# Performance work log

Hardware: AMD Instinct MI355X
Metric: run time of the kernel (lower is better)

## Reference

```python
import jax, jax.numpy as jnp
import numpy as np

N = 50000        # nodes
E = 1_600_000    # edges
IN = 64          # in_feats
H = 128          # h_feats
L = 5            # num_layers
G = 512          # graphs in batch
C = 10           # num_classes


def setup_inputs() -> dict:
    key = jax.random.key(0)
    ks = jax.random.split(key, 12)
    s = 0.05
    x = jax.random.normal(ks[0], (N, IN), jnp.float32)
    edge_index = jax.random.randint(ks[1], (2, E), 0, N, dtype=jnp.int32)
    batch = jnp.sort(jax.random.randint(ks[2], (N,), 0, G, dtype=jnp.int32))
    edge_weight = jax.random.uniform(ks[3], (E,), jnp.float32)
    # GatedGraphConv params: per-layer mixing weight + shared GRUCell
    weight = jax.random.normal(ks[4], (L, H, H), jnp.float32) * s
    w_ih = jax.random.normal(ks[5], (3 * H, H), jnp.float32) * s
    w_hh = jax.random.normal(ks[6], (3 * H, H), jnp.float32) * s
    b_ih = jax.random.normal(ks[7], (3 * H,), jnp.float32) * s
    b_hh = jax.random.normal(ks[8], (3 * H,), jnp.float32) * s
    # MLP head
    dense1_w = jax.random.normal(ks[9], (4 * H, H), jnp.float32) * s
    dense1_b = jnp.zeros((4 * H,), jnp.float32)
    dense2_w = jax.random.normal(ks[10], (C, 4 * H), jnp.float32) * s
    dense2_b = jnp.zeros((C,), jnp.float32)
    return dict(x=x, edge_index=edge_index, batch=batch, edge_weight=edge_weight,
                weight=weight, w_ih=w_ih, w_hh=w_hh, b_ih=b_ih, b_hh=b_hh,
                dense1_w=dense1_w, dense1_b=dense1_b,
                dense2_w=dense2_w, dense2_b=dense2_b)


def _gru_cell(m, h, w_ih, w_hh, b_ih, b_hh):
    # torch.nn.GRUCell(input=m, hidden=h)
    gi = m @ w_ih.T + b_ih
    gh = h @ w_hh.T + b_hh
    i_r, i_z, i_n = jnp.split(gi, 3, axis=-1)
    h_r, h_z, h_n = jnp.split(gh, 3, axis=-1)
    r = jax.nn.sigmoid(i_r + h_r)
    z = jax.nn.sigmoid(i_z + h_z)
    n = jnp.tanh(i_n + r * h_n)
    return (1.0 - z) * n + z * h


def reference(x, edge_index, batch, edge_weight, weight, w_ih, w_hh, b_ih, b_hh,
              dense1_w, dense1_b, dense2_w, dense2_b):
    src, dst = edge_index[0], edge_index[1]
    # pad in_feats -> h_feats (PyG GatedGraphConv)
    h = jnp.pad(x, ((0, 0), (0, H - IN)))
    for l in range(L):
        m = h @ weight[l]                          # [N, H]
        msg = m[src] * edge_weight[:, None]        # gather + edge gating [E, H]
        agg = jax.ops.segment_sum(msg, dst, num_segments=N)  # scatter-add
        h = _gru_cell(agg, h, w_ih, w_hh, b_ih, b_hh)
    pooled = jax.ops.segment_max(h, batch, num_segments=G)   # global max pool [G, H]
    # dropout is identity in eval mode
    hid = jax.nn.relu(pooled @ dense1_w.T + dense1_b)
    out = hid @ dense2_w.T + dense2_b
    return out
```

## Files before the change

### kernel.cpp

```cpp
#include <hip/hip_runtime.h>
#include <hip/hip_bf16.h>

#define NN 50000
#define NE 1600000
#define FIN 64
#define H 128
#define NL 5
#define NG 512
#define NC 10

typedef __attribute__((ext_vector_type(8))) short short8;
typedef __attribute__((ext_vector_type(4))) float f32x4;

#define OFF_H2A   0
#define OFF_H2B   3200000
#define OFF_CUR   6400000
#define OFF_OFF   6450176
#define OFF_CSR   6500352
#define OFF_POOL  8900352
#define OFF_FWF   8965888
#define OFF_FWHH  9088768

__device__ __forceinline__ short rne_bf16(float f){
    unsigned u = __float_as_uint(f);
    unsigned r = (u + 0x7FFFu + ((u >> 16) & 1u)) >> 16;
    return (short)r;
}
__device__ __forceinline__ float bf_lo(unsigned v){ return __uint_as_float(v << 16); }
__device__ __forceinline__ float bf_hi(unsigned v){ return __uint_as_float(v & 0xFFFF0000u); }


__global__ void k_hist(const int* __restrict__ ei, int* __restrict__ cnt){
    int e0 = (blockIdx.x*256 + threadIdx.x)*4;
    if (e0 + 3 < NE){
        int4 d = *(const int4*)(ei + NE + e0);
        atomicAdd(&cnt[d.x], 1); atomicAdd(&cnt[d.y], 1);
        atomicAdd(&cnt[d.z], 1); atomicAdd(&cnt[d.w], 1);
    } else {
        for (int e = e0; e < NE; ++e) atomicAdd(&cnt[ei[NE + e]], 1);
    }
}

__global__ void k_scan(int* __restrict__ cur, int* __restrict__ off){
    __shared__ int s[1024];
    int t = threadIdx.x;
    const int CH = 49;
    int base = t*CH;
    int m = (NN + 1) - base; if (m > CH) m = CH; if (m < 0) m = 0;
    int sum = 0;
    for (int i = 0; i < m; ++i) sum += (cur[base + i] + 15) & ~15;
    s[t] = sum; __syncthreads();
    for (int o = 1; o < 1024; o <<= 1){
        int v = (t >= o) ? s[t - o] : 0; __syncthreads();
        s[t] += v; __syncthreads();
    }
    int run = s[t] - sum;
    for (int i = 0; i < m; ++i){
        int c = (cur[base + i] + 15) & ~15;
        off[base + i] = run;
        cur[base + i] = run;
        run += c;
    }
}

__global__ void k_fill(const int* __restrict__ ei, const float* __restrict__ ew,
                       int* __restrict__ cur, unsigned* __restrict__ csr){
    int e0 = (blockIdx.x*256 + threadIdx.x)*4;
    if (e0 + 3 < NE){
        int4   s = *(const int4*)(ei + e0);
        int4   d = *(const int4*)(ei + NE + e0);
        float4 w = *(const float4*)(ew + e0);
        int p0 = atomicAdd(&cur[d.x], 1);
        int p1 = atomicAdd(&cur[d.y], 1);
        int p2 = atomicAdd(&cur[d.z], 1);
        int p3 = atomicAdd(&cur[d.w], 1);
        csr[p0] = (unsigned)s.x | (((unsigned)(ushort)rne_bf16(w.x)) << 16);
        csr[p1] = (unsigned)s.y | (((unsigned)(ushort)rne_bf16(w.y)) << 16);
        csr[p2] = (unsigned)s.z | (((unsigned)(ushort)rne_bf16(w.z)) << 16);
        csr[p3] = (unsigned)s.w | (((unsigned)(ushort)rne_bf16(w.w)) << 16);
    } else {
        for (int e = e0; e < NE; ++e){
            int src = ei[e], dst = ei[NE + e];
            int pos = atomicAdd(&cur[dst], 1);
            csr[pos] = (unsigned)src | (((unsigned)(ushort)rne_bf16(ew[e])) << 16);
        }
    }
}


__global__ void k_pad(const float* __restrict__ x, ushort* __restrict__ h2a){
    int idx = blockIdx.x*256 + threadIdx.x;
    int n = idx >> 4, f8 = idx & 15;
    short8 v;
    if (f8 < 8){
        float4 a = *(const float4*)(x + n*FIN + f8*8);
        float4 b = *(const float4*)(x + n*FIN + f8*8 + 4);
        v[0]=rne_bf16(a.x); v[1]=rne_bf16(a.y); v[2]=rne_bf16(a.z); v[3]=rne_bf16(a.w);
        v[4]=rne_bf16(b.x); v[5]=rne_bf16(b.y); v[6]=rne_bf16(b.z); v[7]=rne_bf16(b.w);
    } else {
        v[0]=0; v[1]=0; v[2]=0; v[3]=0; v[4]=0; v[5]=0; v[6]=0; v[7]=0;
    }
    *(short8*)(h2a + idx*8) = v;
}

__global__ void k_fuse(const float* __restrict__ W, const float* __restrict__ wih,
                       short* __restrict__ fwf){
    int idx = blockIdx.x*256 + threadIdx.x;
    int l = idx / 49152;
    int r = idx % 49152;
    int k = r / 384, n = r % 384;
    const float4* wl = (const float4*)(W + l*16384 + k*128);
    const float4* wi = (const float4*)(wih + n*128);
    float acc = 0.f;
    #pragma unroll 8
    for (int c = 0; c < 32; ++c){
        float4 a = wl[c], b = wi[c];
        acc += a.x*b.x + a.y*b.y + a.z*b.z + a.w*b.w;
    }
    int lane = ((k>>3)&3)*16 + (n&15);
    fwf[l*49152 + (((n>>4)*4 + (k>>5))*64 + lane)*8 + (k&7)] = rne_bf16(acc);
}

__global__ void k_cvt_whh(const float* __restrict__ whh, short* __restrict__ fwhh){
    int idx = blockIdx.x*256 + threadIdx.x;
    int k = idx / 384, n = idx % 384;
    float v = whh[n*128 + k];
    int lane = ((k>>3)&3)*16 + (n&15);
    fwhh[(((n>>4)*4 + (k>>5))*64 + lane)*8 + (k&7)] = rne_bf16(v);
}

__global__ void k_init_pool(unsigned* __restrict__ p){
    p[blockIdx.x*256 + threadIdx.x] = 0x007FFFFFu;
}

__global__ __launch_bounds__(512)
void k_layer(const ushort* __restrict__ h2r, ushort* __restrict__ h2w,
             const int* __restrict__ off, const unsigned* __restrict__ csr,
             const short* __restrict__ fwf, const short* __restrict__ fwhh,
             const float* __restrict__ b_ih, const float* __restrict__ b_hh,
             const int* __restrict__ batch, unsigned* __restrict__ pooled,
             int last){
    __shared__ ushort tl[16*136];
    int tid = threadIdx.x;
    int n0 = blockIdx.x * 16;
    int wave = tid >> 6, lane = tid & 63;
    int lane_lo = lane & 15, quad = lane >> 4;
    int grp = lane >> 4, fl = lane & 15;

    for (int sub = 0; sub < 2; ++sub){
        int node = n0 + wave*2 + sub;
        int start = __builtin_amdgcn_readfirstlane(off[node]);
        int end   = __builtin_amdgcn_readfirstlane(off[node + 1]);
        float a0=0.f,a1=0.f,a2=0.f,a3=0.f,a4=0.f,a5=0.f,a6=0.f,a7=0.f;
        const ushort* hb = h2r + fl*8;
        for (int i = start; i < end; i += 16){
            uint4 c = *(const uint4*)(csr + i + grp*4);
            uint4 v0 = *(const uint4*)(hb + (c.x & 0xFFFFu)*H);
            uint4 v1 = *(const uint4*)(hb + (c.y & 0xFFFFu)*H);
            uint4 v2 = *(const uint4*)(hb + (c.z & 0xFFFFu)*H);
            uint4 v3 = *(const uint4*)(hb + (c.w & 0xFFFFu)*H);
            float w0 = bf_hi(c.x), w1 = bf_hi(c.y), w2 = bf_hi(c.z), w3 = bf_hi(c.w);
            a0 += w0*bf_lo(v0.x); a1 += w0*bf_hi(v0.x); a2 += w0*bf_lo(v0.y); a3 += w0*bf_hi(v0.y);
            a4 += w0*bf_lo(v0.z); a5 += w0*bf_hi(v0.z); a6 += w0*bf_lo(v0.w); a7 += w0*bf_hi(v0.w);
            a0 += w1*bf_lo(v1.x); a1 += w1*bf_hi(v1.x); a2 += w1*bf_lo(v1.y); a3 += w1*bf_hi(v1.y);
            a4 += w1*bf_lo(v1.z); a5 += w1*bf_hi(v1.z); a6 += w1*bf_lo(v1.w); a7 += w1*bf_hi(v1.w);
            a0 += w2*bf_lo(v2.x); a1 += w2*bf_hi(v2.x); a2 += w2*bf_lo(v2.y); a3 += w2*bf_hi(v2.y);
            a4 += w2*bf_lo(v2.z); a5 += w2*bf_hi(v2.z); a6 += w2*bf_lo(v2.w); a7 += w2*bf_hi(v2.w);
            a0 += w3*bf_lo(v3.x); a1 += w3*bf_hi(v3.x); a2 += w3*bf_lo(v3.y); a3 += w3*bf_hi(v3.y);
            a4 += w3*bf_lo(v3.z); a5 += w3*bf_hi(v3.z); a6 += w3*bf_lo(v3.w); a7 += w3*bf_hi(v3.w);
        }
        a0 += __shfl_xor(a0,16); a1 += __shfl_xor(a1,16); a2 += __shfl_xor(a2,16); a3 += __shfl_xor(a3,16);
        a4 += __shfl_xor(a4,16); a5 += __shfl_xor(a5,16); a6 += __shfl_xor(a6,16); a7 += __shfl_xor(a7,16);
        a0 += __shfl_xor(a0,32); a1 += __shfl_xor(a1,32); a2 += __shfl_xor(a2,32); a3 += __shfl_xor(a3,32);
        a4 += __shfl_xor(a4,32); a5 += __shfl_xor(a5,32); a6 += __shfl_xor(a6,32); a7 += __shfl_xor(a7,32);
        if (lane < 16){
            short8 hbv;
            hbv[0]=rne_bf16(a0); hbv[1]=rne_bf16(a1); hbv[2]=rne_bf16(a2); hbv[3]=rne_bf16(a3);
            hbv[4]=rne_bf16(a4); hbv[5]=rne_bf16(a5); hbv[6]=rne_bf16(a6); hbv[7]=rne_bf16(a7);
            *(short8*)(tl + (wave*2 + sub)*136 + fl*8) = hbv;
        }
    }
    __syncthreads();

    f32x4 ai[3], ah[3];
    #pragma unroll
    for (int i = 0; i < 3; ++i){ ai[i] = (f32x4){0.f,0.f,0.f,0.f}; ah[i] = (f32x4){0.f,0.f,0.f,0.f}; }

    const ushort* arow_t = tl + lane_lo*136;
    const ushort* arow_h = h2r + (size_t)(n0 + lane_lo)*H;
    #pragma unroll
    for (int kt = 0; kt < 4; ++kt){
        short8 at  = *(const short8*)(arow_t + kt*32 + quad*8);
        short8 ahh = *(const short8*)(arow_h + kt*32 + quad*8);
        #pragma unroll
        for (int s = 0; s < 3; ++s){
            int tile = (s*8 + wave)*4 + kt;
            short8 bi = *(const short8*)(fwf  + tile*512 + lane*8);
            short8 bh = *(const short8*)(fwhh + tile*512 + lane*8);
            ai[s] = __builtin_amdgcn_mfma_f32_16x16x32_bf16(at,  bi, ai[s], 0, 0, 0);
            ah[s] = __builtin_amdgcn_mfma_f32_16x16x32_bf16(ahh, bh, ah[s], 0, 0, 0);
        }
    }

    {
        int j = wave*16 + lane_lo;
        float bir = b_ih[j], biz = b_ih[128 + j], bin_ = b_ih[256 + j];
        float bhr = b_hh[j], bhz = b_hh[128 + j], bhn  = b_hh[256 + j];
        #pragma unroll
        for (int r = 0; r < 4; ++r){
            int row = n0 + quad*4 + r;
            float gir = ai[0][r] + bir, ghr = ah[0][r] + bhr;
            float giz = ai[1][r] + biz, ghz = ah[1][r] + bhz;
            float gin = ai[2][r] + bin_, ghn = ah[2][r] + bhn;
            float rr = 1.f/(1.f + __expf(-(gir + ghr)));
            float zz = 1.f/(1.f + __expf(-(giz + ghz)));
            float nn = tanhf(gin + rr*ghn);
            float ho = __uint_as_float(((unsigned)h2r[(size_t)row*H + j]) << 16);
            float hv = (1.f - zz)*nn + zz*ho;
            if (!last){
                h2w[(size_t)row*H + j] = (ushort)rne_bf16(hv);
            } else {
                int g = batch[row];
                unsigned u = __float_as_uint(hv);
                u = (u & 0x80000000u) ? ~u : (u | 0x80000000u);
                atomicMax(pooled + g*H + j, u);
            }
        }
    }
}


__global__ void k_head(const unsigned* __restrict__ pooled,
                       const float* __restrict__ d1w, const float* __restrict__ d1b,
                       const float* __restrict__ d2w, const float* __restrict__ d2b,
                       float* __restrict__ out){
    __shared__ float sp[128];
    __shared__ float shid[512];
    int g = blockIdx.x, tid = threadIdx.x;
    if (tid < 128){
        unsigned u = pooled[g*H + tid];
        sp[tid] = __uint_as_float((u & 0x80000000u) ? (u ^ 0x80000000u) : ~u);
    }
    __syncthreads();
    for (int o = tid; o < 512; o += 256){
        float acc = d1b[o];
        for (int k = 0; k < H; ++k) acc += sp[k] * d1w[o*H + k];
        shid[o] = fmaxf(acc, 0.f);
    }
    __syncthreads();
    if (tid < NC){
        float acc = d2b[tid];
        for (int o = 0; o < 512; ++o) acc += shid[o] * d2w[tid*512 + o];
        out[g*NC + tid] = acc;
    }
}

extern "C" void kernel_launch(void* const* d_in, const int* in_sizes, int n_in,
                              void* d_out, int out_size, void* d_ws, size_t ws_size,
                              hipStream_t stream){
    const float* x     = (const float*)d_in[0];
    const int*   ei    = (const int*)d_in[1];
    const int*   batch = (const int*)d_in[2];
    const float* ew    = (const float*)d_in[3];
    const float* W     = (const float*)d_in[4];
    const float* wih   = (const float*)d_in[5];
    const float* whh   = (const float*)d_in[6];
    const float* bih   = (const float*)d_in[7];
    const float* bhh   = (const float*)d_in[8];
    const float* d1w   = (const float*)d_in[9];
    const float* d1b   = (const float*)d_in[10];
    const float* d2w   = (const float*)d_in[11];
    const float* d2b   = (const float*)d_in[12];
    float* out = (float*)d_out;

    float*  ws  = (float*)d_ws;
    ushort* h2a = (ushort*)(ws + OFF_H2A);
    ushort* h2b = (ushort*)(ws + OFF_H2B);
    int*    cur = (int*)(ws + OFF_CUR);
    int*    off = (int*)(ws + OFF_OFF);
    unsigned* csr = (unsigned*)(ws + OFF_CSR);
    unsigned* pooled = (unsigned*)(ws + OFF_POOL);
    short*  fwf  = (short*)(ws + OFF_FWF);
    short*  fwhh = (short*)(ws + OFF_FWHH);

    hipMemsetAsync(cur, 0, 50176*sizeof(int), stream);
    hipMemsetAsync(csr, 0, 2400000*sizeof(unsigned), stream);
    k_hist<<<1563, 256, 0, stream>>>(ei, cur);
    k_scan<<<1, 1024, 0, stream>>>(cur, off);
    k_fill<<<1563, 256, 0, stream>>>(ei, ew, cur, csr);

    k_fuse<<<960, 256, 0, stream>>>(W, wih, fwf);
    k_cvt_whh<<<192, 256, 0, stream>>>(whh, fwhh);
    k_pad<<<3125, 256, 0, stream>>>(x, h2a);
    k_init_pool<<<256, 256, 0, stream>>>(pooled);

    for (int l = 0; l < NL; ++l){
        ushort* h2r = (l & 1) ? h2b : h2a;
        ushort* h2w = (l & 1) ? h2a : h2b;
        k_layer<<<3125, 512, 0, stream>>>(h2r, h2w, off, csr,
                                          fwf + (size_t)l*49152, fwhh, bih, bhh,
                                          batch, pooled, (l == NL-1) ? 1 : 0);
    }

    k_head<<<NG, 256, 0, stream>>>(pooled, d1w, d1b, d2w, d2b, out);
}
```

Before: 871.8 us.

## Bucket CSR edges per destination by source chunk for gather locality

Each destination's edge list is split into 6 sub-segments keyed by source-index range (src>>13), so neighbour gathers in the layer kernel walk the feature table one chunk at a time. The aim is to keep the 2 MB slice of h that concurrent waves touch resident in L2 instead of scattering over the whole table. Segment padding drops from 16 to 4 edges, and a bounds guard handles partial 16-edge steps. The trade-off is more short inner loops, with more serial iterations, divergence and segment-offset loads per node. The counters and pool buffer now alias the ping-pong feature region, and pool initialisation moves to just before the final layer.

```diff
diff --git a/kernel.cpp b/kernel.cpp
--- a/kernel.cpp
+++ b/kernel.cpp
@@ -8,16 +8,18 @@
 #define NL 5
 #define NG 512
 #define NC 10
+#define NCH 6
+#define NSEG (NN*NCH)
 
 typedef __attribute__((ext_vector_type(8))) short short8;
 typedef __attribute__((ext_vector_type(4))) float f32x4;
 
 #define OFF_H2A   0
 #define OFF_H2B   3200000
-#define OFF_CUR   6400000
-#define OFF_OFF   6450176
-#define OFF_CSR   6500352
-#define OFF_POOL  8900352
+#define OFF_CUR   3200000
+#define OFF_POOL  3200000
+#define OFF_OFF   6400000
+#define OFF_CSR   6700064
 #define OFF_FWF   8965888
 #define OFF_FWHH  9088768
 
@@ -28,27 +30,32 @@
 }
 __device__ __forceinline__ float bf_lo(unsigned v){ return __uint_as_float(v << 16); }
 __device__ __forceinline__ float bf_hi(unsigned v){ return __uint_as_float(v & 0xFFFF0000u); }
+__device__ __forceinline__ int chk(int s){ int c = s >> 13; return c > (NCH-1) ? (NCH-1) : c; }
 
 
 __global__ void k_hist(const int* __restrict__ ei, int* __restrict__ cnt){
     int e0 = (blockIdx.x*256 + threadIdx.x)*4;
     if (e0 + 3 < NE){
+        int4 s = *(const int4*)(ei + e0);
         int4 d = *(const int4*)(ei + NE + e0);
-        atomicAdd(&cnt[d.x], 1); atomicAdd(&cnt[d.y], 1);
-        atomicAdd(&cnt[d.z], 1); atomicAdd(&cnt[d.w], 1);
+        atomicAdd(&cnt[d.x*NCH + chk(s.x)], 1);
+        atomicAdd(&cnt[d.y*NCH + chk(s.y)], 1);
+        atomicAdd(&cnt[d.z*NCH + chk(s.z)], 1);
+        atomicAdd(&cnt[d.w*NCH + chk(s.w)], 1);
     } else {
-        for (int e = e0; e < NE; ++e) atomicAdd(&cnt[ei[NE + e]], 1);
+        for (int e = e0; e < NE; ++e)
+            atomicAdd(&cnt[ei[NE + e]*NCH + chk(ei[e])], 1);
     }
 }
 
 __global__ void k_scan(int* __restrict__ cur, int* __restrict__ off){
     __shared__ int s[1024];
     int t = threadIdx.x;
-    const int CH = 49;
+    const int CH = 294;
     int base = t*CH;
-    int m = (NN + 1) - base; if (m > CH) m = CH; if (m < 0) m = 0;
+    int m = (NSEG + 1) - base; if (m > CH) m = CH; if (m < 0) m = 0;
     int sum = 0;
-    for (int i = 0; i < m; ++i) sum += (cur[base + i] + 15) & ~15;
+    for (int i = 0; i < m; ++i) sum += (cur[base + i] + 3) & ~3;
     s[t] = sum; __syncthreads();
     for (int o = 1; o < 1024; o <<= 1){
         int v = (t >= o) ? s[t - o] : 0; __syncthreads();
@@ -56,7 +63,7 @@
     }
     int run = s[t] - sum;
     for (int i = 0; i < m; ++i){
-        int c = (cur[base + i] + 15) & ~15;
+        int c = (cur[base + i] + 3) & ~3;
         off[base + i] = run;
         cur[base + i] = run;
         run += c;
@@ -70,10 +77,10 @@
         int4   s = *(const int4*)(ei + e0);
         int4   d = *(const int4*)(ei + NE + e0);
         float4 w = *(const float4*)(ew + e0);
-        int p0 = atomicAdd(&cur[d.x], 1);
-        int p1 = atomicAdd(&cur[d.y], 1);
-        int p2 = atomicAdd(&cur[d.z], 1);
-        int p3 = atomicAdd(&cur[d.w], 1);
+        int p0 = atomicAdd(&cur[d.x*NCH + chk(s.x)], 1);
+        int p1 = atomicAdd(&cur[d.y*NCH + chk(s.y)], 1);
+        int p2 = atomicAdd(&cur[d.z*NCH + chk(s.z)], 1);
+        int p3 = atomicAdd(&cur[d.w*NCH + chk(s.w)], 1);
         csr[p0] = (unsigned)s.x | (((unsigned)(ushort)rne_bf16(w.x)) << 16);
         csr[p1] = (unsigned)s.y | (((unsigned)(ushort)rne_bf16(w.y)) << 16);
         csr[p2] = (unsigned)s.z | (((unsigned)(ushort)rne_bf16(w.z)) << 16);
@@ -81,7 +88,7 @@
     } else {
         for (int e = e0; e < NE; ++e){
             int src = ei[e], dst = ei[NE + e];
-            int pos = atomicAdd(&cur[dst], 1);
+            int pos = atomicAdd(&cur[dst*NCH + chk(src)], 1);
             csr[pos] = (unsigned)src | (((unsigned)(ushort)rne_bf16(ew[e])) << 16);
         }
     }
@@ -149,25 +156,31 @@
 
     for (int sub = 0; sub < 2; ++sub){
         int node = n0 + wave*2 + sub;
-        int start = __builtin_amdgcn_readfirstlane(off[node]);
-        int end   = __builtin_amdgcn_readfirstlane(off[node + 1]);
+        int s6 = node*NCH;
         float a0=0.f,a1=0.f,a2=0.f,a3=0.f,a4=0.f,a5=0.f,a6=0.f,a7=0.f;
         const ushort* hb = h2r + fl*8;
-        for (int i = start; i < end; i += 16){
-            uint4 c = *(const uint4*)(csr + i + grp*4);
-            uint4 v0 = *(const uint4*)(hb + (c.x & 0xFFFFu)*H);
-            uint4 v1 = *(const uint4*)(hb + (c.y & 0xFFFFu)*H);
-            uint4 v2 = *(const uint4*)(hb + (c.z & 0xFFFFu)*H);
-            uint4 v3 = *(const uint4*)(hb + (c.w & 0xFFFFu)*H);
-            float w0 = bf_hi(c.x), w1 = bf_hi(c.y), w2 = bf_hi(c.z), w3 = bf_hi(c.w);
-            a0 += w0*bf_lo(v0.x); a1 += w0*bf_hi(v0.x); a2 += w0*bf_lo(v0.y); a3 += w0*bf_hi(v0.y);
-            a4 += w0*bf_lo(v0.z); a5 += w0*bf_hi(v0.z); a6 += w0*bf_lo(v0.w); a7 += w0*bf_hi(v0.w);
-            a0 += w1*bf_lo(v1.x); a1 += w1*bf_hi(v1.x); a2 += w1*bf_lo(v1.y); a3 += w1*bf_hi(v1.y);
-            a4 += w1*bf_lo(v1.z); a5 += w1*bf_hi(v1.z); a6 += w1*bf_lo(v1.w); a7 += w1*bf_hi(v1.w);
-            a0 += w2*bf_lo(v2.x); a1 += w2*bf_hi(v2.x); a2 += w2*bf_lo(v2.y); a3 += w2*bf_hi(v2.y);
-            a4 += w2*bf_lo(v2.z); a5 += w2*bf_hi(v2.z); a6 += w2*bf_lo(v2.w); a7 += w2*bf_hi(v2.w);
-            a0 += w3*bf_lo(v3.x); a1 += w3*bf_hi(v3.x); a2 += w3*bf_lo(v3.y); a3 += w3*bf_hi(v3.y);
-            a4 += w3*bf_lo(v3.z); a5 += w3*bf_hi(v3.z); a6 += w3*bf_lo(v3.w); a7 += w3*bf_hi(v3.w);
+        for (int c = 0; c < NCH; ++c){
+            int start = __builtin_amdgcn_readfirstlane(off[s6 + c]);
+            int end   = __builtin_amdgcn_readfirstlane(off[s6 + c + 1]);
+            for (int i = start; i < end; i += 16){
+                int ii = i + grp*4;
+                if (ii < end){
+                    uint4 cq = *(const uint4*)(csr + ii);
+                    uint4 v0 = *(const uint4*)(hb + (cq.x & 0xFFFFu)*H);
+                    uint4 v1 = *(const uint4*)(hb + (cq.y & 0xFFFFu)*H);
+                    uint4 v2 = *(const uint4*)(hb + (cq.z & 0xFFFFu)*H);
+                    uint4 v3 = *(const uint4*)(hb + (cq.w & 0xFFFFu)*H);
+                    float w0 = bf_hi(cq.x), w1 = bf_hi(cq.y), w2 = bf_hi(cq.z), w3 = bf_hi(cq.w);
+                    a0 += w0*bf_lo(v0.x); a1 += w0*bf_hi(v0.x); a2 += w0*bf_lo(v0.y); a3 += w0*bf_hi(v0.y);
+                    a4 += w0*bf_lo(v0.z); a5 += w0*bf_hi(v0.z); a6 += w0*bf_lo(v0.w); a7 += w0*bf_hi(v0.w);
+                    a0 += w1*bf_lo(v1.x); a1 += w1*bf_hi(v1.x); a2 += w1*bf_lo(v1.y); a3 += w1*bf_hi(v1.y);
+                    a4 += w1*bf_lo(v1.z); a5 += w1*bf_hi(v1.z); a6 += w1*bf_lo(v1.w); a7 += w1*bf_hi(v1.w);
+                    a0 += w2*bf_lo(v2.x); a1 += w2*bf_hi(v2.x); a2 += w2*bf_lo(v2.y); a3 += w2*bf_hi(v2.y);
+                    a4 += w2*bf_lo(v2.z); a5 += w2*bf_hi(v2.z); a6 += w2*bf_lo(v2.w); a7 += w2*bf_hi(v2.w);
+                    a0 += w3*bf_lo(v3.x); a1 += w3*bf_hi(v3.x); a2 += w3*bf_lo(v3.y); a3 += w3*bf_hi(v3.y);
+                    a4 += w3*bf_lo(v3.z); a5 += w3*bf_hi(v3.z); a6 += w3*bf_lo(v3.w); a7 += w3*bf_hi(v3.w);
+                }
+            }
         }
         a0 += __shfl_xor(a0,16); a1 += __shfl_xor(a1,16); a2 += __shfl_xor(a2,16); a3 += __shfl_xor(a3,16);
         a4 += __shfl_xor(a4,16); a5 += __shfl_xor(a5,16); a6 += __shfl_xor(a6,16); a7 += __shfl_xor(a7,16);
@@ -277,14 +290,14 @@
     ushort* h2a = (ushort*)(ws + OFF_H2A);
     ushort* h2b = (ushort*)(ws + OFF_H2B);
     int*    cur = (int*)(ws + OFF_CUR);
+    unsigned* pooled = (unsigned*)(ws + OFF_POOL);
     int*    off = (int*)(ws + OFF_OFF);
     unsigned* csr = (unsigned*)(ws + OFF_CSR);
-    unsigned* pooled = (unsigned*)(ws + OFF_POOL);
     short*  fwf  = (short*)(ws + OFF_FWF);
     short*  fwhh = (short*)(ws + OFF_FWHH);
 
-    hipMemsetAsync(cur, 0, 50176*sizeof(int), stream);
-    hipMemsetAsync(csr, 0, 2400000*sizeof(unsigned), stream);
+    hipMemsetAsync(cur, 0, (NSEG + 1)*sizeof(int), stream);
+    hipMemsetAsync(csr, 0, 2265824*sizeof(unsigned), stream);
     k_hist<<<1563, 256, 0, stream>>>(ei, cur);
     k_scan<<<1, 1024, 0, stream>>>(cur, off);
     k_fill<<<1563, 256, 0, stream>>>(ei, ew, cur, csr);
@@ -292,11 +305,11 @@
     k_fuse<<<960, 256, 0, stream>>>(W, wih, fwf);
     k_cvt_whh<<<192, 256, 0, stream>>>(whh, fwhh);
     k_pad<<<3125, 256, 0, stream>>>(x, h2a);
-    k_init_pool<<<256, 256, 0, stream>>>(pooled);
 
     for (int l = 0; l < NL; ++l){
         ushort* h2r = (l & 1) ? h2b : h2a;
         ushort* h2w = (l & 1) ? h2a : h2b;
+        if (l == NL-1) k_init_pool<<<256, 256, 0, stream>>>(pooled);
         k_layer<<<3125, 512, 0, stream>>>(h2r, h2w, off, csr,
                                           fwf + (size_t)l*49152, fwhh, bih, bhh,
                                           batch, pooled, (l == NL-1) ? 1 : 0);
```

New measurement: 1.650 ms. 1.89x slower.
